# Kernel optimization log

Hardware: AMD Instinct MI355X
Metric: run time of the kernel (lower is better)

## Reference

```python
import jax, jax.numpy as jnp
import numpy as np

IN_F = 256
OUT_F = 256
ALPHA = 0.2  # LeakyReLU negative slope
NEG_INF = -9e15


def setup_inputs() -> dict:
    key = jax.random.key(0)
    k_h, k_adj, k_w, k_a = jax.random.split(key, 4)
    N = 8192
    h = jax.random.normal(k_h, (N, IN_F), dtype=jnp.float32)
    adj = jax.random.randint(k_adj, (N, N), 0, 2, dtype=jnp.int32)
    # xavier_uniform with gain=1.414
    gain = 1.414
    limW = gain * np.sqrt(6.0 / (IN_F + OUT_F))
    W = jax.random.uniform(k_w, (IN_F, OUT_F), minval=-limW, maxval=limW, dtype=jnp.float32)
    lima = gain * np.sqrt(6.0 / (2 * OUT_F + 1))
    a = jax.random.uniform(k_a, (2 * OUT_F, 1), minval=-lima, maxval=lima, dtype=jnp.float32)
    return {"h": h, "adj": adj, "W": W, "a": a}


def reference(h, adj, W, a):
    # Wh: [N, F]
    Wh = h @ W
    # The original materializes [N, N, 2F] concat pairs; equivalently
    # e[i, j] = leakyrelu(Wh[i] . a[:F] + Wh[j] . a[F:])
    a1 = a[:OUT_F, 0]  # [F]
    a2 = a[OUT_F:, 0]  # [F]
    s1 = Wh @ a1       # [N]
    s2 = Wh @ a2       # [N]
    e = jax.nn.leaky_relu(s1[:, None] + s2[None, :], negative_slope=ALPHA)  # [N, N]
    att = jnp.where(adj > 0, e, NEG_INF)
    att = jax.nn.softmax(att, axis=1)
    # dropout p=0.0 (eval) -> identity
    h_prime = att @ Wh  # [N, F]
    return jax.nn.elu(h_prime)  # concat=True path
```

## Files before the change

### kernel.cpp

```cpp
#include <hip/hip_runtime.h>

#define NN 8192
#define FF 256
#define PST 136

typedef _Float16 h8 __attribute__((ext_vector_type(8)));
typedef _Float16 h4 __attribute__((ext_vector_type(4)));
typedef float    f4 __attribute__((ext_vector_type(4)));
typedef int      i4v __attribute__((ext_vector_type(4)));

__device__ __forceinline__ unsigned fenc(float x) {
  unsigned u = __float_as_uint(x);
  return (u & 0x80000000u) ? ~u : (u | 0x80000000u);
}
__device__ __forceinline__ float fdec(unsigned e) {
  unsigned u = (e & 0x80000000u) ? (e ^ 0x80000000u) : ~e;
  return __uint_as_float(u);
}

__device__ __forceinline__ void sync_lds() {
  __builtin_amdgcn_s_waitcnt(0xc07f);
  __builtin_amdgcn_s_barrier();
}

__global__ __launch_bounds__(256) void k_wh(
    const float* __restrict__ h, const float* __restrict__ W,
    const float* __restrict__ a, _Float16* __restrict__ wfrag,
    float* __restrict__ s1, _Float16* __restrict__ s2h,
    unsigned* __restrict__ s2maxe) {
  __shared__ float hs[16 * 256];
  __shared__ _Float16 whs[16 * 264];
  const int t = threadIdx.x;
  const int r0 = blockIdx.x * 16;
#pragma unroll
  for (int i = 0; i < 4; ++i) {
    int idx = i * 1024 + t * 4;
    *(f4*)&hs[idx] = *(const f4*)&h[(size_t)r0 * 256 + idx];
  }
  __syncthreads();
  const int lane = t & 63;
  const int wv = t >> 6;
  const int rg = wv * 4;
  const int c4 = lane * 4;
  float acc[4][4];
#pragma unroll
  for (int i = 0; i < 4; ++i)
#pragma unroll
    for (int k = 0; k < 4; ++k) acc[i][k] = 0.f;
  f4 w[8];
#pragma unroll
  for (int i = 0; i < 8; ++i) w[i] = *(const f4*)&W[i * 256 + c4];
  for (int f = 0; f < 256; f += 8) {
    f4 nw[8];
    if (f < 248) {
#pragma unroll
      for (int i = 0; i < 8; ++i) nw[i] = *(const f4*)&W[(f + 8 + i) * 256 + c4];
    }
#pragma unroll
    for (int i = 0; i < 4; ++i) {
      f4 h0 = *(const f4*)&hs[(rg + i) * 256 + f];
      f4 h1 = *(const f4*)&hs[(rg + i) * 256 + f + 4];
#pragma unroll
      for (int k = 0; k < 4; ++k)
        acc[i][k] += h0[0]*w[0][k] + h0[1]*w[1][k] + h0[2]*w[2][k] + h0[3]*w[3][k]
                   + h1[0]*w[4][k] + h1[1]*w[5][k] + h1[2]*w[6][k] + h1[3]*w[7][k];
    }
    if (f < 248) {
#pragma unroll
      for (int i = 0; i < 8; ++i) w[i] = nw[i];
    }
  }
  float a1v[4], a2v[4];
#pragma unroll
  for (int k = 0; k < 4; ++k) { a1v[k] = a[c4 + k]; a2v[k] = a[256 + c4 + k]; }
#pragma unroll
  for (int i = 0; i < 4; ++i) {
    h4 hh;
    float p1 = 0.f, p2 = 0.f;
#pragma unroll
    for (int k = 0; k < 4; ++k) {
      hh[k] = (_Float16)acc[i][k];
      p1 += acc[i][k] * a1v[k];
      p2 += acc[i][k] * a2v[k];
    }
    *(h4*)&whs[(rg + i) * 264 + c4] = hh;
#pragma unroll
    for (int off = 32; off; off >>= 1) {
      p1 += __shfl_xor(p1, off);
      p2 += __shfl_xor(p2, off);
    }
    if (lane == 0) {
      const int r = r0 + rg + i;
      s1[r] = p1;
      s2h[r] = (_Float16)p2;
      atomicMax(s2maxe, fenc(p2));
    }
  }
  __syncthreads();
  {
    const int kt = blockIdx.x >> 1;
    const int hb = blockIdx.x & 1;
    const int lp = hb * 32 + (t & 31);
    const int kb = ((t & 31) >> 4) * 8;
    const int m16e = t & 15;
#pragma unroll
    for (int p = 0; p < 2; ++p) {
      const int n = (t >> 5) + p * 8;
      h8 v;
#pragma unroll
      for (int j = 0; j < 8; ++j) v[j] = whs[(kb + j) * 264 + n * 16 + m16e];
      *(h8*)&wfrag[(((size_t)kt * 16 + n) << 9) + lp * 8] = v;
    }
  }
}

__global__ __launch_bounds__(512, 2) void k_gat(
    const int* __restrict__ adj, const _Float16* __restrict__ wfrag,
    const float* __restrict__ s1g, const _Float16* __restrict__ s2h,
    const unsigned* __restrict__ s2maxe,
    float* __restrict__ o0, float* __restrict__ o1,
    float* __restrict__ o2, float* __restrict__ o3,
    float* __restrict__ lbuf) {
  __shared__ _Float16 P[2][128 * PST];
  __shared__ _Float16 s2l[2048];
  const int t = threadIdx.x;
  const int lane = t & 63;
  const int w = t >> 6;
  const int q = lane >> 4;
  const int m16 = lane & 15;
  const int rt = (int)blockIdx.x >> 2;
  const int kq = (int)blockIdx.x & 3;
  const int r0 = rt * 128;

  if (t < 256) ((h8*)s2l)[t] = ((const h8*)(s2h + kq * 2048))[t];

  const int rloc = w * 16 + m16;
  const float s2m = fdec(*s2maxe);
  const float s1r = s1g[r0 + rloc];
  const float u0 = s1r + s2m;
  const float mi = fmaxf(u0, 0.2f * u0);
  const float s1mi = s1r - mi;

  f4 acc[8][2];
#pragma unroll
  for (int mt = 0; mt < 8; ++mt)
#pragma unroll
    for (int n = 0; n < 2; ++n)
#pragma unroll
      for (int e = 0; e < 4; ++e) acc[mt][n][e] = 0.f;
  float lsum = 0.f;

  const int* adjp = adj + (size_t)(r0 + rloc) * NN + kq * 2048 + q * 8;
  __syncthreads();

  i4v adjc[8], adjn[8];
#pragma unroll
  for (int ks = 0; ks < 4; ++ks) {
    adjc[2 * ks]     = __builtin_nontemporal_load((const i4v*)(adjp + ks * 32));
    adjc[2 * ks + 1] = __builtin_nontemporal_load((const i4v*)(adjp + ks * 32 + 4));
  }

  for (int p = 0; p < 16; ++p) {
    const int kb = kq * 64 + p * 4;
    h8 bb[8];
#pragma unroll
    for (int ks = 0; ks < 4; ++ks) {
      const _Float16* wfb =
          wfrag + (((size_t)(kb + ks) * 16 + 2 * w) << 9) + lane * 8;
      bb[2 * ks]     = *(const h8*)(wfb);
      bb[2 * ks + 1] = *(const h8*)(wfb + 512);
    }
    if (p < 15) {
#pragma unroll
      for (int ks = 0; ks < 4; ++ks) {
        adjn[2 * ks]     = __builtin_nontemporal_load(
            (const i4v*)(adjp + (p + 1) * 128 + ks * 32));
        adjn[2 * ks + 1] = __builtin_nontemporal_load(
            (const i4v*)(adjp + (p + 1) * 128 + ks * 32 + 4));
      }
    }
    _Float16* Pb = &P[p & 1][0];
#pragma unroll
    for (int ks = 0; ks < 4; ++ks) {
      const h8 s2c = *(const h8*)&s2l[p * 128 + ks * 32 + q * 8];
      const i4v a0 = adjc[2 * ks];
      const i4v a1 = adjc[2 * ks + 1];
      h8 pa;
#pragma unroll
      for (int j = 0; j < 8; ++j) {
        const float s2v = (float)s2c[j];
        const float u = s1r + s2v;
        const float arg = s1mi + s2v - 0.8f * fminf(u, 0.f);
        const int msk = (j < 4) ? a0[j] : a1[j - 4];
        const float pv = (msk > 0) ? __expf(arg) : 0.f;
        lsum += pv;
        pa[j] = (_Float16)pv;
      }
      *(h8*)&Pb[rloc * PST + ks * 32 + q * 8] = pa;
    }
    sync_lds();
#pragma unroll
    for (int ks = 0; ks < 4; ++ks) {
#pragma unroll
      for (int mt = 0; mt < 8; ++mt) {
        const h8 A = *(const h8*)&Pb[(mt * 16 + m16) * PST + ks * 32 + q * 8];
        acc[mt][0] = __builtin_amdgcn_mfma_f32_16x16x32_f16(A, bb[2*ks],   acc[mt][0], 0, 0, 0);
        acc[mt][1] = __builtin_amdgcn_mfma_f32_16x16x32_f16(A, bb[2*ks+1], acc[mt][1], 0, 0, 0);
      }
    }
#pragma unroll
    for (int i = 0; i < 8; ++i) adjc[i] = adjn[i];
  }

  lsum += __shfl_xor(lsum, 16);
  lsum += __shfl_xor(lsum, 32);
  if (q == 0) lbuf[kq * NN + r0 + rloc] = lsum;

  float* ob = (kq == 0) ? o0 : (kq == 1) ? o1 : (kq == 2) ? o2 : o3;
#pragma unroll
  for (int mt = 0; mt < 8; ++mt)
#pragma unroll
    for (int n = 0; n < 2; ++n)
#pragma unroll
      for (int v = 0; v < 4; ++v)
        ob[(size_t)(r0 + mt * 16 + q * 4 + v) * FF + w * 32 + n * 16 + m16] =
            acc[mt][n][v];
}

__global__ __launch_bounds__(256) void k_fin(
    float* __restrict__ out, const float* __restrict__ o1,
    const float* __restrict__ o2, const float* __restrict__ o3,
    const float* __restrict__ lbuf) {
  const int t = threadIdx.x;
  const int row = blockIdx.x * 16 + (t >> 4);
  const int c0 = (t & 15) * 16;
  const float linv = 1.0f / (lbuf[row] + lbuf[NN + row] +
                             lbuf[2 * NN + row] + lbuf[3 * NN + row]);
#pragma unroll
  for (int i = 0; i < 4; ++i) {
    const size_t off = (size_t)row * FF + c0 + i * 4;
    f4 v0 = *(const f4*)&out[off];
    f4 v1 = *(const f4*)&o1[off];
    f4 v2 = *(const f4*)&o2[off];
    f4 v3 = *(const f4*)&o3[off];
    f4 o;
#pragma unroll
    for (int e = 0; e < 4; ++e) {
      float x = (v0[e] + v1[e] + v2[e] + v3[e]) * linv;
      o[e] = (x > 0.f) ? x : (__expf(x) - 1.f);
    }
    *(f4*)&out[off] = o;
  }
}

extern "C" void kernel_launch(void* const* d_in, const int* in_sizes, int n_in,
                              void* d_out, int out_size, void* d_ws, size_t ws_size,
                              hipStream_t stream) {
  const float* h   = (const float*)d_in[0];
  const int*   adj = (const int*)d_in[1];
  const float* W   = (const float*)d_in[2];
  const float* a   = (const float*)d_in[3];
  float* out = (float*)d_out;

  char* ws = (char*)d_ws;
  _Float16* wfrag = (_Float16*)ws;
  float*    o1    = (float*)(ws + (4u << 20));
  float*    o2    = (float*)(ws + (12u << 20));
  float*    o3    = (float*)(ws + (20u << 20));
  float*    lbuf  = (float*)(ws + (28u << 20));
  unsigned* s2me  = (unsigned*)(ws + (28u << 20) + 131072);
  float*    s1    = (float*)(ws + (28u << 20) + 131136);
  _Float16* s2h   = (_Float16*)(ws + (28u << 20) + 131136 + 32768);

  hipMemsetAsync(s2me, 0, 4, stream);
  k_wh<<<512, 256, 0, stream>>>(h, W, a, wfrag, s1, s2h, s2me);
  k_gat<<<256, 512, 0, stream>>>(adj, wfrag, s1, s2h, s2me,
                                 out, o1, o2, o3, lbuf);
  k_fin<<<512, 256, 0, stream>>>(out, o1, o2, o3, lbuf);
}
```

Measured before the change: 514.9 us.

## Feed P directly from registers into MFMA, dropping LDS staging and barriers

```diff
diff --git a/kernel.cpp b/kernel.cpp
--- a/kernel.cpp
+++ b/kernel.cpp
@@ -2,7 +2,6 @@
 
 #define NN 8192
 #define FF 256
-#define PST 136
 
 typedef _Float16 h8 __attribute__((ext_vector_type(8)));
 typedef _Float16 h4 __attribute__((ext_vector_type(4)));
@@ -16,11 +15,6 @@
 __device__ __forceinline__ float fdec(unsigned e) {
   unsigned u = (e & 0x80000000u) ? (e ^ 0x80000000u) : ~e;
   return __uint_as_float(u);
-}
-
-__device__ __forceinline__ void sync_lds() {
-  __builtin_amdgcn_s_waitcnt(0xc07f);
-  __builtin_amdgcn_s_barrier();
 }
 
 __global__ __launch_bounds__(256) void k_wh(
@@ -114,14 +108,13 @@
   }
 }
 
-__global__ __launch_bounds__(512, 2) void k_gat(
+__global__ __launch_bounds__(256, 2) void k_gat(
     const int* __restrict__ adj, const _Float16* __restrict__ wfrag,
     const float* __restrict__ s1g, const _Float16* __restrict__ s2h,
     const unsigned* __restrict__ s2maxe,
     float* __restrict__ o0, float* __restrict__ o1,
     float* __restrict__ o2, float* __restrict__ o3,
     float* __restrict__ lbuf) {
-  __shared__ _Float16 P[2][128 * PST];
   __shared__ _Float16 s2l[2048];
   const int t = threadIdx.x;
   const int lane = t & 63;
@@ -130,101 +123,80 @@
   const int m16 = lane & 15;
   const int rt = (int)blockIdx.x >> 2;
   const int kq = (int)blockIdx.x & 3;
-  const int r0 = rt * 128;
-
-  if (t < 256) ((h8*)s2l)[t] = ((const h8*)(s2h + kq * 2048))[t];
-
-  const int rloc = w * 16 + m16;
+  const int r0 = rt * 64;
+
+  ((h8*)s2l)[t] = ((const h8*)(s2h + kq * 2048))[t];
+
+  const int srow = w * 16 + m16;
   const float s2m = fdec(*s2maxe);
-  const float s1r = s1g[r0 + rloc];
+  const float s1r = s1g[r0 + srow];
   const float u0 = s1r + s2m;
   const float mi = fmaxf(u0, 0.2f * u0);
   const float s1mi = s1r - mi;
 
-  f4 acc[8][2];
-#pragma unroll
-  for (int mt = 0; mt < 8; ++mt)
-#pragma unroll
-    for (int n = 0; n < 2; ++n)
-#pragma unroll
-      for (int e = 0; e < 4; ++e) acc[mt][n][e] = 0.f;
+  f4 acc[16];
+#pragma unroll
+  for (int n = 0; n < 16; ++n)
+#pragma unroll
+    for (int e = 0; e < 4; ++e) acc[n][e] = 0.f;
   float lsum = 0.f;
 
-  const int* adjp = adj + (size_t)(r0 + rloc) * NN + kq * 2048 + q * 8;
+  const int* adjp = adj + (size_t)(r0 + srow) * NN + kq * 2048 + q * 8;
   __syncthreads();
 
-  i4v adjc[8], adjn[8];
-#pragma unroll
-  for (int ks = 0; ks < 4; ++ks) {
-    adjc[2 * ks]     = __builtin_nontemporal_load((const i4v*)(adjp + ks * 32));
-    adjc[2 * ks + 1] = __builtin_nontemporal_load((const i4v*)(adjp + ks * 32 + 4));
-  }
-
-  for (int p = 0; p < 16; ++p) {
-    const int kb = kq * 64 + p * 4;
-    h8 bb[8];
-#pragma unroll
-    for (int ks = 0; ks < 4; ++ks) {
-      const _Float16* wfb =
-          wfrag + (((size_t)(kb + ks) * 16 + 2 * w) << 9) + lane * 8;
-      bb[2 * ks]     = *(const h8*)(wfb);
-      bb[2 * ks + 1] = *(const h8*)(wfb + 512);
-    }
-    if (p < 15) {
-#pragma unroll
-      for (int ks = 0; ks < 4; ++ks) {
-        adjn[2 * ks]     = __builtin_nontemporal_load(
-            (const i4v*)(adjp + (p + 1) * 128 + ks * 32));
-        adjn[2 * ks + 1] = __builtin_nontemporal_load(
-            (const i4v*)(adjp + (p + 1) * 128 + ks * 32 + 4));
-      }
-    }
-    _Float16* Pb = &P[p & 1][0];
-#pragma unroll
-    for (int ks = 0; ks < 4; ++ks) {
-      const h8 s2c = *(const h8*)&s2l[p * 128 + ks * 32 + q * 8];
-      const i4v a0 = adjc[2 * ks];
-      const i4v a1 = adjc[2 * ks + 1];
-      h8 pa;
-#pragma unroll
-      for (int j = 0; j < 8; ++j) {
-        const float s2v = (float)s2c[j];
-        const float u = s1r + s2v;
-        const float arg = s1mi + s2v - 0.8f * fminf(u, 0.f);
-        const int msk = (j < 4) ? a0[j] : a1[j - 4];
-        const float pv = (msk > 0) ? __expf(arg) : 0.f;
-        lsum += pv;
-        pa[j] = (_Float16)pv;
-      }
-      *(h8*)&Pb[rloc * PST + ks * 32 + q * 8] = pa;
-    }
-    sync_lds();
-#pragma unroll
-    for (int ks = 0; ks < 4; ++ks) {
-#pragma unroll
-      for (int mt = 0; mt < 8; ++mt) {
-        const h8 A = *(const h8*)&Pb[(mt * 16 + m16) * PST + ks * 32 + q * 8];
-        acc[mt][0] = __builtin_amdgcn_mfma_f32_16x16x32_f16(A, bb[2*ks],   acc[mt][0], 0, 0, 0);
-        acc[mt][1] = __builtin_amdgcn_mfma_f32_16x16x32_f16(A, bb[2*ks+1], acc[mt][1], 0, 0, 0);
-      }
-    }
-#pragma unroll
-    for (int i = 0; i < 8; ++i) adjc[i] = adjn[i];
+  i4v c0 = __builtin_nontemporal_load((const i4v*)(adjp));
+  i4v c1 = __builtin_nontemporal_load((const i4v*)(adjp + 4));
+  i4v d0 = __builtin_nontemporal_load((const i4v*)(adjp + 32));
+  i4v d1 = __builtin_nontemporal_load((const i4v*)(adjp + 36));
+
+#pragma unroll 1
+  for (int kt = 0; kt < 64; ++kt) {
+    const _Float16* wfb =
+        wfrag + (((size_t)(kq * 64 + kt) * 16) << 9) + lane * 8;
+    h8 bb[16];
+#pragma unroll
+    for (int n = 0; n < 16; ++n) bb[n] = *(const h8*)(wfb + (n << 9));
+    i4v e0 = d0, e1 = d1;
+    if (kt < 62) {
+      e0 = __builtin_nontemporal_load((const i4v*)(adjp + (kt + 2) * 32));
+      e1 = __builtin_nontemporal_load((const i4v*)(adjp + (kt + 2) * 32 + 4));
+    }
+    const h8 s2c = *(const h8*)&s2l[kt * 32 + q * 8];
+    h8 pa;
+#pragma unroll
+    for (int j = 0; j < 4; ++j) {
+      const float s2v = (float)s2c[j];
+      const float u = s1r + s2v;
+      const float arg = s1mi + s2v - 0.8f * fminf(u, 0.f);
+      const float pv = (c0[j] > 0) ? __expf(arg) : 0.f;
+      lsum += pv;
+      pa[j] = (_Float16)pv;
+    }
+#pragma unroll
+    for (int j = 0; j < 4; ++j) {
+      const float s2v = (float)s2c[4 + j];
+      const float u = s1r + s2v;
+      const float arg = s1mi + s2v - 0.8f * fminf(u, 0.f);
+      const float pv = (c1[j] > 0) ? __expf(arg) : 0.f;
+      lsum += pv;
+      pa[4 + j] = (_Float16)pv;
+    }
+#pragma unroll
+    for (int n = 0; n < 16; ++n)
+      acc[n] = __builtin_amdgcn_mfma_f32_16x16x32_f16(pa, bb[n], acc[n], 0, 0, 0);
+    c0 = d0; c1 = d1; d0 = e0; d1 = e1;
   }
 
   lsum += __shfl_xor(lsum, 16);
   lsum += __shfl_xor(lsum, 32);
-  if (q == 0) lbuf[kq * NN + r0 + rloc] = lsum;
+  if (q == 0) lbuf[kq * NN + r0 + srow] = lsum;
 
   float* ob = (kq == 0) ? o0 : (kq == 1) ? o1 : (kq == 2) ? o2 : o3;
 #pragma unroll
-  for (int mt = 0; mt < 8; ++mt)
-#pragma unroll
-    for (int n = 0; n < 2; ++n)
-#pragma unroll
-      for (int v = 0; v < 4; ++v)
-        ob[(size_t)(r0 + mt * 16 + q * 4 + v) * FF + w * 32 + n * 16 + m16] =
-            acc[mt][n][v];
+  for (int n = 0; n < 16; ++n)
+#pragma unroll
+    for (int v = 0; v < 4; ++v)
+      ob[(size_t)(r0 + w * 16 + q * 4 + v) * FF + n * 16 + m16] = acc[n][v];
 }
 
 __global__ __launch_bounds__(256) void k_fin(
@@ -274,7 +246,7 @@
 
   hipMemsetAsync(s2me, 0, 4, stream);
   k_wh<<<512, 256, 0, stream>>>(h, W, a, wfrag, s1, s2h, s2me);
-  k_gat<<<256, 512, 0, stream>>>(adj, wfrag, s1, s2h, s2me,
+  k_gat<<<512, 256, 0, stream>>>(adj, wfrag, s1, s2h, s2me,
                                  out, o1, o2, o3, lbuf);
   k_fin<<<512, 256, 0, stream>>>(out, o1, o2, o3, lbuf);
 }
```

New measurement: 580.9 us. +12.8%, slower.
